# Performance work log

Measured on AMD Instinct MI355X. Metric: run time of the kernel, lower is better.

The kernel has to match this reference:

```python
import jax, jax.numpy as jnp
import numpy as np

DIM = 768
HEADS = 12
DH = DIM // HEADS
HIDDEN = 4 * DIM
EPS = 1e-5


def layernorm(x, g, b):
    mu = jnp.mean(x, axis=-1, keepdims=True)
    var = jnp.mean(jnp.square(x - mu), axis=-1, keepdims=True)
    return (x - mu) * jax.lax.rsqrt(var + EPS) * g + b


def setup_inputs() -> dict:
    key = jax.random.key(0)
    ks = jax.random.split(key, 12)
    B, N = 8, 1024
    s_in = 1.0 / np.sqrt(DIM)
    s_hid = 1.0 / np.sqrt(HIDDEN)
    return {
        "x": jax.random.normal(ks[0], (B, N, DIM), jnp.float32),
        "q_extra": jax.random.normal(ks[1], (B, N, DIM), jnp.float32),
        "ln1_g": jnp.ones((DIM,), jnp.float32),
        "ln1_b": jnp.zeros((DIM,), jnp.float32),
        "w_kv": jax.random.normal(ks[2], (DIM, 2 * DIM), jnp.float32) * s_in,
        "w_out": jax.random.normal(ks[3], (DIM, DIM), jnp.float32) * s_in,
        "b_out": jnp.zeros((DIM,), jnp.float32),
        "ln2_g": jnp.ones((DIM,), jnp.float32),
        "ln2_b": jnp.zeros((DIM,), jnp.float32),
        "w1": jax.random.normal(ks[4], (DIM, HIDDEN), jnp.float32) * s_in,
        "b1": jnp.zeros((HIDDEN,), jnp.float32),
        "w2": jax.random.normal(ks[5], (HIDDEN, DIM), jnp.float32) * s_hid,
        "b2": jnp.zeros((DIM,), jnp.float32),
    }


def reference(x, q_extra, ln1_g, ln1_b, w_kv, w_out, b_out, ln2_g, ln2_b, w1, b1, w2, b2):
    B, N, C = x.shape
    scale = DH ** (-0.5)

    # pre-norm cross attention
    xn = layernorm(x, ln1_g, ln1_b)
    kv = (xn @ w_kv).reshape(B, N, 2, HEADS, DH)
    k = kv[:, :, 0]  # [B,N,H,Dh]
    v = kv[:, :, 1]
    q = q_extra.reshape(B, N, HEADS, DH)
    dots = jnp.einsum('bnhd,bmhd->bhnm', q, k) * scale
    attn = jax.nn.softmax(dots, axis=-1)
    out = jnp.einsum('bhnm,bmhd->bnhd', attn, v).reshape(B, N, C)
    out = out @ w_out + b_out

    x = x + out  # residual

    # pre-norm MLP
    h = layernorm(x, ln2_g, ln2_b)
    h = jax.nn.gelu(h @ w1 + b1, approximate=False)
    h = h @ w2 + b2
    return x + h
```

## Files before the change

### kernel.cpp

```cpp
#include <hip/hip_runtime.h>

typedef __attribute__((ext_vector_type(8))) short short8;
typedef __attribute__((ext_vector_type(8))) _Float16 half8;
typedef __attribute__((ext_vector_type(2))) __fp16 fp16x2;
typedef __attribute__((ext_vector_type(4))) float float4v;

__device__ __forceinline__ unsigned short f2bf(float f) {
  union { unsigned int i; float f; } x; x.f = f;
  unsigned int r = x.i + 0x7fffu + ((x.i >> 16) & 1u);
  return (unsigned short)(r >> 16);
}

__global__ void ln_kernel(const float* __restrict__ in, const float* __restrict__ g,
                          const float* __restrict__ b, unsigned short* __restrict__ out) {
  const int row = blockIdx.x, t = threadIdx.x;
  const float* xr = in + (size_t)row * 768;
  float v0 = xr[t], v1 = xr[t + 256], v2 = xr[t + 512];
  float s = v0 + v1 + v2;
  float s2 = v0 * v0 + v1 * v1 + v2 * v2;
  for (int off = 32; off > 0; off >>= 1) {
    s += __shfl_xor(s, off, 64);
    s2 += __shfl_xor(s2, off, 64);
  }
  __shared__ float red[8];
  const int wave = t >> 6, lane = t & 63;
  if (lane == 0) { red[wave] = s; red[wave + 4] = s2; }
  __syncthreads();
  s = red[0] + red[1] + red[2] + red[3];
  s2 = red[4] + red[5] + red[6] + red[7];
  const float mu = s * (1.0f / 768.0f);
  const float var = s2 * (1.0f / 768.0f) - mu * mu;
  const float rstd = rsqrtf(var + 1e-5f);
  unsigned short* orow = out + (size_t)row * 768;
  orow[t]       = f2bf((v0 - mu) * rstd * g[t]       + b[t]);
  orow[t + 256] = f2bf((v1 - mu) * rstd * g[t + 256] + b[t + 256]);
  orow[t + 512] = f2bf((v2 - mu) * rstd * g[t + 512] + b[t + 512]);
}

__global__ void wtrans_kernel(const float* __restrict__ in, unsigned short* __restrict__ out,
                              int K, int N) {
  __shared__ float tile[32][33];
  const int k0 = blockIdx.y * 32, n0 = blockIdx.x * 32;
  const int tr = threadIdx.x >> 5, tc = threadIdx.x & 31;
#pragma unroll
  for (int i = 0; i < 4; ++i)
    tile[tr + i * 8][tc] = in[(size_t)(k0 + tr + i * 8) * N + n0 + tc];
  __syncthreads();
#pragma unroll
  for (int i = 0; i < 4; ++i)
    out[(size_t)(n0 + tr + i * 8) * K + k0 + tc] = f2bf(tile[tc][tr + i * 8]);
}

__device__ __forceinline__ void gemm128(
    const unsigned short* __restrict__ A, int lda,
    const unsigned short* __restrict__ Bt, int ldb, int K,
    int row0, int col0,
    unsigned short* As, unsigned short* Bs,
    float4v acc[4][4]) {
  const int t = threadIdx.x, lane = t & 63, wave = t >> 6;
  const int quad = lane >> 4, l16 = lane & 15;
  const int wr = wave >> 1, wc = wave & 1;
  const int sr = lane >> 2;
  const int sc = (lane & 3) * 8;
#pragma unroll
  for (int mt = 0; mt < 4; ++mt)
#pragma unroll
    for (int nt = 0; nt < 4; ++nt) acc[mt][nt] = (float4v)(0.0f);

  for (int kk = 0; kk < K; kk += 32) {
    __syncthreads();
#pragma unroll
    for (int j = 0; j < 2; ++j) {
      const int chunk = wave * 2 + j;
      const int r = chunk * 16 + sr;
      __builtin_amdgcn_global_load_lds(
          (const __attribute__((address_space(1))) unsigned int*)(A + (size_t)(row0 + r) * lda + kk + sc),
          (__attribute__((address_space(3))) unsigned int*)(As + chunk * 512),
          16, 0, 0);
      __builtin_amdgcn_global_load_lds(
          (const __attribute__((address_space(1))) unsigned int*)(Bt + (size_t)(col0 + r) * ldb + kk + sc),
          (__attribute__((address_space(3))) unsigned int*)(Bs + chunk * 512),
          16, 0, 0);
    }
    __syncthreads();
    short8 af[4], bfv[4];
#pragma unroll
    for (int i = 0; i < 4; ++i) {
      af[i]  = *(const short8*)(As + (wr * 64 + i * 16 + l16) * 32 + quad * 8);
      bfv[i] = *(const short8*)(Bs + (wc * 64 + i * 16 + l16) * 32 + quad * 8);
    }
#pragma unroll
    for (int mt = 0; mt < 4; ++mt)
#pragma unroll
      for (int nt = 0; nt < 4; ++nt)
        acc[mt][nt] = __builtin_amdgcn_mfma_f32_16x16x32_bf16(af[mt], bfv[nt], acc[mt][nt], 0, 0, 0);
  }
}

#define GEMM128_PROLOGUE                                         \
  __shared__ unsigned short As[128 * 32];                        \
  __shared__ unsigned short Bs[128 * 32];                        \
  float4v acc[4][4];                                             \
  const int col0 = blockIdx.x * 128, row0 = blockIdx.y * 128;    \
  const int t = threadIdx.x, lane = t & 63, wave = t >> 6;       \
  const int quad = lane >> 4, l16 = lane & 15;                   \
  const int wr = wave >> 1, wc = wave & 1; (void)t;

__device__ __forceinline__ void gemm12864(
    const unsigned short* __restrict__ A, int lda,
    const unsigned short* __restrict__ Bt, int ldb, int K,
    int row0, int col0,
    unsigned short* As, unsigned short* Bs,
    float4v acc[2][4]) {
  const int t = threadIdx.x, lane = t & 63, wave = t >> 6;
  const int quad = lane >> 4, l16 = lane & 15;
  const int sr = lane >> 2;
  const int sc = (lane & 3) * 8;
#pragma unroll
  for (int mt = 0; mt < 2; ++mt)
#pragma unroll
    for (int nt = 0; nt < 4; ++nt) acc[mt][nt] = (float4v)(0.0f);

  for (int kk = 0; kk < K; kk += 32) {
    __syncthreads();
#pragma unroll
    for (int j = 0; j < 2; ++j) {
      const int chunk = wave * 2 + j;
      const int r = chunk * 16 + sr;
      __builtin_amdgcn_global_load_lds(
          (const __attribute__((address_space(1))) unsigned int*)(A + (size_t)(row0 + r) * lda + kk + sc),
          (__attribute__((address_space(3))) unsigned int*)(As + chunk * 512),
          16, 0, 0);
    }
    {
      const int r = wave * 16 + sr;
      __builtin_amdgcn_global_load_lds(
          (const __attribute__((address_space(1))) unsigned int*)(Bt + (size_t)(col0 + r) * ldb + kk + sc),
          (__attribute__((address_space(3))) unsigned int*)(Bs + wave * 512),
          16, 0, 0);
    }
    __syncthreads();
    short8 af[2], bfv[4];
#pragma unroll
    for (int i = 0; i < 2; ++i)
      af[i] = *(const short8*)(As + (wave * 32 + i * 16 + l16) * 32 + quad * 8);
#pragma unroll
    for (int i = 0; i < 4; ++i)
      bfv[i] = *(const short8*)(Bs + (i * 16 + l16) * 32 + quad * 8);
#pragma unroll
    for (int mt = 0; mt < 2; ++mt)
#pragma unroll
      for (int nt = 0; nt < 4; ++nt)
        acc[mt][nt] = __builtin_amdgcn_mfma_f32_16x16x32_bf16(af[mt], bfv[nt], acc[mt][nt], 0, 0, 0);
  }
}

#define GEMM12864_PROLOGUE                                       \
  __shared__ unsigned short As[128 * 32];                        \
  __shared__ unsigned short Bs[64 * 32];                         \
  float4v acc[2][4];                                             \
  const int col0 = blockIdx.x * 64, row0 = blockIdx.y * 128;     \
  const int t = threadIdx.x, lane = t & 63, wave = t >> 6;       \
  const int quad = lane >> 4, l16 = lane & 15; (void)t;

__global__ void gemm_kv_kernel(const unsigned short* __restrict__ xn,
                               const unsigned short* __restrict__ wkvt,
                               _Float16* __restrict__ kbuf,
                               _Float16* __restrict__ vtbuf) {
  GEMM128_PROLOGUE
  gemm128(xn, 768, wkvt, 768, 768, row0, col0, As, Bs, acc);
#pragma unroll
  for (int mt = 0; mt < 4; ++mt)
#pragma unroll
    for (int nt = 0; nt < 4; ++nt) {
      const int j = col0 + wc * 64 + nt * 16 + l16;
#pragma unroll
      for (int r = 0; r < 4; ++r) {
        const int m = row0 + wr * 64 + mt * 16 + quad * 4 + r;
        const int bb = m >> 10, n = m & 1023;
        const float c = acc[mt][nt][r];
        if (j < 768) {
          const int hh = j >> 6, d = j & 63;
          kbuf[((size_t)(bb * 12 + hh) * 1024 + n) * 64 + d] = (_Float16)c;
        } else {
          const int j2 = j - 768, hh = j2 >> 6, d = j2 & 63;
          vtbuf[((size_t)(bb * 12 + hh) * 64 + d) * 1024 + n] = (_Float16)c;
        }
      }
    }
}

#define AST 72
#define PST 72
__global__ void attn_kernel(const float* __restrict__ q_extra,
                            const _Float16* __restrict__ kbuf,
                            const _Float16* __restrict__ vtbuf,
                            unsigned short* __restrict__ ao) {
  __shared__ _Float16 Ks[64 * AST];
  __shared__ _Float16 Vs[64 * AST];
  __shared__ _Float16 Ps[4][2][16 * PST];
  const int b = blockIdx.z, h = blockIdx.y, q0 = blockIdx.x * 128;
  const int t = threadIdx.x, lane = t & 63, wave = t >> 6;
  const int quad = lane >> 4, l16 = lane & 15;

  half8 qf[2][2];
#pragma unroll
  for (int qt = 0; qt < 2; ++qt) {
    const float* qp = q_extra +
        ((size_t)((b * 1024 + q0 + qt * 64 + wave * 16 + l16) * 12 + h)) * 64 + quad * 8;
    float4 a0 = *(const float4*)(qp);
    float4 a1 = *(const float4*)(qp + 4);
    float4 c0 = *(const float4*)(qp + 32);
    float4 c1 = *(const float4*)(qp + 36);
    union { fp16x2 h2[4]; half8 h8; } u0, u1;
    u0.h2[0] = __builtin_amdgcn_cvt_pkrtz(a0.x * 0.125f, a0.y * 0.125f);
    u0.h2[1] = __builtin_amdgcn_cvt_pkrtz(a0.z * 0.125f, a0.w * 0.125f);
    u0.h2[2] = __builtin_amdgcn_cvt_pkrtz(a1.x * 0.125f, a1.y * 0.125f);
    u0.h2[3] = __builtin_amdgcn_cvt_pkrtz(a1.z * 0.125f, a1.w * 0.125f);
    u1.h2[0] = __builtin_amdgcn_cvt_pkrtz(c0.x * 0.125f, c0.y * 0.125f);
    u1.h2[1] = __builtin_amdgcn_cvt_pkrtz(c0.z * 0.125f, c0.w * 0.125f);
    u1.h2[2] = __builtin_amdgcn_cvt_pkrtz(c1.x * 0.125f, c1.y * 0.125f);
    u1.h2[3] = __builtin_amdgcn_cvt_pkrtz(c1.z * 0.125f, c1.w * 0.125f);
    qf[qt][0] = u0.h8; qf[qt][1] = u1.h8;
  }

  const _Float16* kb = kbuf + (size_t)(b * 12 + h) * 65536;
  const _Float16* vb = vtbuf + (size_t)(b * 12 + h) * 65536;
  const int srow = t >> 2, su = (t & 3) * 16;

  half8 kp0 = *(const half8*)(kb + (size_t)srow * 64 + su);
  half8 kp1 = *(const half8*)(kb + (size_t)srow * 64 + su + 8);
  half8 vp0 = *(const half8*)(vb + (size_t)srow * 1024 + su);
  half8 vp1 = *(const half8*)(vb + (size_t)srow * 1024 + su + 8);

  float m_s[2] = {-1e30f, -1e30f}, l_s[2] = {0.f, 0.f};
  float4v acc[2][4];
#pragma unroll
  for (int qt = 0; qt < 2; ++qt)
#pragma unroll
    for (int nt = 0; nt < 4; ++nt) acc[qt][nt] = (float4v)(0.f);

  for (int c = 0; c < 16; ++c) {
    __syncthreads();
    *(half8*)(Ks + srow * AST + su)     = kp0;
    *(half8*)(Ks + srow * AST + su + 8) = kp1;
    *(half8*)(Vs + srow * AST + su)     = vp0;
    *(half8*)(Vs + srow * AST + su + 8) = vp1;
    if (c < 15) {
      const int key1 = (c + 1) * 64;
      kp0 = *(const half8*)(kb + (size_t)(key1 + srow) * 64 + su);
      kp1 = *(const half8*)(kb + (size_t)(key1 + srow) * 64 + su + 8);
      vp0 = *(const half8*)(vb + (size_t)srow * 1024 + key1 + su);
      vp1 = *(const half8*)(vb + (size_t)srow * 1024 + key1 + su + 8);
    }
    __syncthreads();

    float4v s[2][4];
#pragma unroll
    for (int kt = 0; kt < 4; ++kt) {
      const _Float16* kr = Ks + (kt * 16 + l16) * AST;
      half8 kf0 = *(const half8*)(kr + quad * 8);
      half8 kf1 = *(const half8*)(kr + 32 + quad * 8);
#pragma unroll
      for (int qt = 0; qt < 2; ++qt) {
        float4v a = (float4v)(0.f);
        a = __builtin_amdgcn_mfma_f32_16x16x32_f16(kf0, qf[qt][0], a, 0, 0, 0);
        a = __builtin_amdgcn_mfma_f32_16x16x32_f16(kf1, qf[qt][1], a, 0, 0, 0);
        s[qt][kt] = a;
      }
    }

    float ab[2][4];
#pragma unroll
    for (int qt = 0; qt < 2; ++qt) {
      float mx = fmaxf(fmaxf(fmaxf(s[qt][0][0], s[qt][0][1]), fmaxf(s[qt][0][2], s[qt][0][3])),
                       fmaxf(fmaxf(s[qt][1][0], s[qt][1][1]), fmaxf(s[qt][1][2], s[qt][1][3])));
      mx = fmaxf(mx, fmaxf(fmaxf(fmaxf(s[qt][2][0], s[qt][2][1]), fmaxf(s[qt][2][2], s[qt][2][3])),
                           fmaxf(fmaxf(s[qt][3][0], s[qt][3][1]), fmaxf(s[qt][3][2], s[qt][3][3]))));
      mx = fmaxf(mx, __shfl_xor(mx, 16, 64));
      mx = fmaxf(mx, __shfl_xor(mx, 32, 64));
      const float mn = fmaxf(m_s[qt], mx);
      const float alpha = __expf(m_s[qt] - mn);
      m_s[qt] = mn;
      _Float16* pw = Ps[wave][qt];
      float sum = 0.0f;
#pragma unroll
      for (int kt = 0; kt < 4; ++kt) {
        const float p0 = __expf(s[qt][kt][0] - mn);
        const float p1 = __expf(s[qt][kt][1] - mn);
        const float p2 = __expf(s[qt][kt][2] - mn);
        const float p3 = __expf(s[qt][kt][3] - mn);
        sum += (p0 + p1) + (p2 + p3);
        union { fp16x2 h2[2]; uint2 u; } pk;
        pk.h2[0] = __builtin_amdgcn_cvt_pkrtz(p0, p1);
        pk.h2[1] = __builtin_amdgcn_cvt_pkrtz(p2, p3);
        *(uint2*)(pw + l16 * PST + kt * 16 + quad * 4) = pk.u;
      }
      sum += __shfl_xor(sum, 16, 64);
      sum += __shfl_xor(sum, 32, 64);
      l_s[qt] = l_s[qt] * alpha + sum;
#pragma unroll
      for (int r = 0; r < 4; ++r) ab[qt][r] = __shfl(alpha, quad * 4 + r, 64);
#pragma unroll
      for (int nt = 0; nt < 4; ++nt)
#pragma unroll
        for (int r = 0; r < 4; ++r) acc[qt][nt][r] *= ab[qt][r];
    }

    half8 pf[2][2];
#pragma unroll
    for (int qt = 0; qt < 2; ++qt) {
      const _Float16* pw = Ps[wave][qt];
      pf[qt][0] = *(const half8*)(pw + l16 * PST + quad * 8);
      pf[qt][1] = *(const half8*)(pw + l16 * PST + 32 + quad * 8);
    }
#pragma unroll
    for (int nt = 0; nt < 4; ++nt) {
      const _Float16* vr = Vs + (nt * 16 + l16) * AST;
      half8 vf0 = *(const half8*)(vr + quad * 8);
      half8 vf1 = *(const half8*)(vr + 32 + quad * 8);
#pragma unroll
      for (int qt = 0; qt < 2; ++qt) {
        acc[qt][nt] = __builtin_amdgcn_mfma_f32_16x16x32_f16(pf[qt][0], vf0, acc[qt][nt], 0, 0, 0);
        acc[qt][nt] = __builtin_amdgcn_mfma_f32_16x16x32_f16(pf[qt][1], vf1, acc[qt][nt], 0, 0, 0);
      }
    }
  }

#pragma unroll
  for (int qt = 0; qt < 2; ++qt) {
    const float inv = 1.0f / l_s[qt];
    float ib[4];
#pragma unroll
    for (int r = 0; r < 4; ++r) ib[r] = __shfl(inv, quad * 4 + r, 64);
#pragma unroll
    for (int nt = 0; nt < 4; ++nt) {
#pragma unroll
      for (int r = 0; r < 4; ++r) {
        const int m = q0 + qt * 64 + wave * 16 + quad * 4 + r;
        ao[(size_t)(b * 1024 + m) * 768 + h * 64 + nt * 16 + l16] =
            f2bf(acc[qt][nt][r] * ib[r]);
      }
    }
  }
}

__global__ void gemm_outproj_kernel(const unsigned short* __restrict__ ao,
                                    const unsigned short* __restrict__ woutt,
                                    const float* __restrict__ b_out,
                                    const float* __restrict__ x,
                                    float* __restrict__ x2) {
  GEMM12864_PROLOGUE
  gemm12864(ao, 768, woutt, 768, 768, row0, col0, As, Bs, acc);
#pragma unroll
  for (int mt = 0; mt < 2; ++mt)
#pragma unroll
    for (int nt = 0; nt < 4; ++nt) {
      const int j = col0 + nt * 16 + l16;
#pragma unroll
      for (int r = 0; r < 4; ++r) {
        const int m = row0 + wave * 32 + mt * 16 + quad * 4 + r;
        const size_t idx = (size_t)m * 768 + j;
        x2[idx] = acc[mt][nt][r] + b_out[j] + x[idx];
      }
    }
}

__global__ void gemm_mlp1_kernel(const unsigned short* __restrict__ h,
                                 const unsigned short* __restrict__ w1t,
                                 const float* __restrict__ b1,
                                 unsigned short* __restrict__ h1) {
  GEMM128_PROLOGUE
  gemm128(h, 768, w1t, 768, 768, row0, col0, As, Bs, acc);
#pragma unroll
  for (int mt = 0; mt < 4; ++mt)
#pragma unroll
    for (int nt = 0; nt < 4; ++nt) {
      const int j = col0 + wc * 64 + nt * 16 + l16;
#pragma unroll
      for (int r = 0; r < 4; ++r) {
        const int m = row0 + wr * 64 + mt * 16 + quad * 4 + r;
        const float y = acc[mt][nt][r] + b1[j];
        const float ge = 0.5f * y * (1.0f + erff(y * 0.70710678118654752f));
        h1[(size_t)m * 3072 + j] = f2bf(ge);
      }
    }
}

__global__ void gemm_mlp2_kernel(const unsigned short* __restrict__ h1,
                                 const unsigned short* __restrict__ w2t,
                                 const float* __restrict__ b2,
                                 const float* __restrict__ x2,
                                 float* __restrict__ out) {
  GEMM12864_PROLOGUE
  gemm12864(h1, 3072, w2t, 3072, 3072, row0, col0, As, Bs, acc);
#pragma unroll
  for (int mt = 0; mt < 2; ++mt)
#pragma unroll
    for (int nt = 0; nt < 4; ++nt) {
      const int j = col0 + nt * 16 + l16;
#pragma unroll
      for (int r = 0; r < 4; ++r) {
        const int m = row0 + wave * 32 + mt * 16 + quad * 4 + r;
        const size_t idx = (size_t)m * 768 + j;
        out[idx] = acc[mt][nt][r] + b2[j] + x2[idx];
      }
    }
}

extern "C" void kernel_launch(void* const* d_in, const int* in_sizes, int n_in,
                              void* d_out, int out_size, void* d_ws, size_t ws_size,
                              hipStream_t stream) {
  const float* x       = (const float*)d_in[0];
  const float* q_extra = (const float*)d_in[1];
  const float* ln1_g   = (const float*)d_in[2];
  const float* ln1_b   = (const float*)d_in[3];
  const float* w_kv    = (const float*)d_in[4];
  const float* w_out   = (const float*)d_in[5];
  const float* b_out   = (const float*)d_in[6];
  const float* ln2_g   = (const float*)d_in[7];
  const float* ln2_b   = (const float*)d_in[8];
  const float* w1      = (const float*)d_in[9];
  const float* b1      = (const float*)d_in[10];
  const float* w2      = (const float*)d_in[11];
  const float* b2      = (const float*)d_in[12];
  float* out = (float*)d_out;

  char* ws = (char*)d_ws;
  unsigned short* xn    = (unsigned short*)(ws);
  _Float16*       kbuf  = (_Float16*)(ws + 12582912);
  _Float16*       vtbuf = (_Float16*)(ws + 25165824);
  unsigned short* ao    = (unsigned short*)(ws + 37748736);
  float*          x2    = (float*)(ws + 50331648);
  unsigned short* h1    = (unsigned short*)(ws + 75497472);
  unsigned short* hbuf  = xn;
  unsigned short* wkvt  = ao;
  unsigned short* woutt = h1;
  unsigned short* w1t   = (unsigned short*)kbuf;
  unsigned short* w2t   = (unsigned short*)vtbuf;

  ln_kernel<<<8192, 256, 0, stream>>>(x, ln1_g, ln1_b, xn);
  wtrans_kernel<<<dim3(48, 24), 256, 0, stream>>>(w_kv, wkvt, 768, 1536);
  wtrans_kernel<<<dim3(24, 24), 256, 0, stream>>>(w_out, woutt, 768, 768);
  gemm_kv_kernel<<<dim3(12, 64), 256, 0, stream>>>(xn, wkvt, kbuf, vtbuf);
  attn_kernel<<<dim3(8, 12, 8), 256, 0, stream>>>(q_extra, kbuf, vtbuf, ao);
  wtrans_kernel<<<dim3(96, 24), 256, 0, stream>>>(w1, w1t, 768, 3072);
  wtrans_kernel<<<dim3(24, 96), 256, 0, stream>>>(w2, w2t, 3072, 768);
  gemm_outproj_kernel<<<dim3(12, 64), 256, 0, stream>>>(ao, woutt, b_out, x, x2);
  ln_kernel<<<8192, 256, 0, stream>>>(x2, ln2_g, ln2_b, hbuf);
  gemm_mlp1_kernel<<<dim3(24, 64), 256, 0, stream>>>(hbuf, w1t, b1, h1);
  gemm_mlp2_kernel<<<dim3(12, 64), 256, 0, stream>>>(h1, w2t, b2, x2, out);
}
```

Before: 429.4 us.

## Deepen GEMM K-tile to 64, XOR-swizzle LDS, and remap blocks per XCD

The GEMM helpers now stage 64-wide K tiles instead of 32, which halves the number of barrier-separated loop iterations. LDS columns are XOR-swizzled by row so the fragment reads avoid bank conflicts. All GEMM launches move to 1D grids, and a swizzle maps consecutive block IDs on the same XCD to contiguous row bands, aiming for better L2 reuse. Shared memory per block doubles, which may reduce occupancy.

Measured after the change: 389.7 us. 9.3% less time.

```diff
diff --git a/kernel.cpp b/kernel.cpp
--- a/kernel.cpp
+++ b/kernel.cpp
@@ -51,6 +51,13 @@
     out[(size_t)(n0 + tr + i * 8) * K + k0 + tc] = f2bf(tile[tc][tr + i * 8]);
 }
 
+#define SWIZ_BLOCK(GX, TW)                                        \
+  const int _id = (int)blockIdx.x;                                \
+  const int _gy8 = (int)gridDim.x / (8 * (GX));                   \
+  const int _xcd = _id & 7, _jj = _id >> 3;                       \
+  const int row0 = (_xcd * _gy8 + _jj / (GX)) * 128;              \
+  const int col0 = (_jj % (GX)) * (TW);
+
 __device__ __forceinline__ void gemm128(
     const unsigned short* __restrict__ A, int lda,
     const unsigned short* __restrict__ Bt, int ldb, int K,
@@ -60,48 +67,52 @@
   const int t = threadIdx.x, lane = t & 63, wave = t >> 6;
   const int quad = lane >> 4, l16 = lane & 15;
   const int wr = wave >> 1, wc = wave & 1;
-  const int sr = lane >> 2;
-  const int sc = (lane & 3) * 8;
+  const int srow = lane >> 3;
+  const int scol = ((lane & 7) ^ srow) * 8;
 #pragma unroll
   for (int mt = 0; mt < 4; ++mt)
 #pragma unroll
     for (int nt = 0; nt < 4; ++nt) acc[mt][nt] = (float4v)(0.0f);
 
-  for (int kk = 0; kk < K; kk += 32) {
-    __syncthreads();
-#pragma unroll
-    for (int j = 0; j < 2; ++j) {
-      const int chunk = wave * 2 + j;
-      const int r = chunk * 16 + sr;
+  for (int kk = 0; kk < K; kk += 64) {
+    __syncthreads();
+#pragma unroll
+    for (int j = 0; j < 4; ++j) {
+      const int chunk = wave * 4 + j;
+      const int r = chunk * 8 + srow;
       __builtin_amdgcn_global_load_lds(
-          (const __attribute__((address_space(1))) unsigned int*)(A + (size_t)(row0 + r) * lda + kk + sc),
+          (const __attribute__((address_space(1))) unsigned int*)(A + (size_t)(row0 + r) * lda + kk + scol),
           (__attribute__((address_space(3))) unsigned int*)(As + chunk * 512),
           16, 0, 0);
       __builtin_amdgcn_global_load_lds(
-          (const __attribute__((address_space(1))) unsigned int*)(Bt + (size_t)(col0 + r) * ldb + kk + sc),
+          (const __attribute__((address_space(1))) unsigned int*)(Bt + (size_t)(col0 + r) * ldb + kk + scol),
           (__attribute__((address_space(3))) unsigned int*)(Bs + chunk * 512),
           16, 0, 0);
     }
     __syncthreads();
-    short8 af[4], bfv[4];
-#pragma unroll
-    for (int i = 0; i < 4; ++i) {
-      af[i]  = *(const short8*)(As + (wr * 64 + i * 16 + l16) * 32 + quad * 8);
-      bfv[i] = *(const short8*)(Bs + (wc * 64 + i * 16 + l16) * 32 + quad * 8);
-    }
-#pragma unroll
-    for (int mt = 0; mt < 4; ++mt)
-#pragma unroll
-      for (int nt = 0; nt < 4; ++nt)
-        acc[mt][nt] = __builtin_amdgcn_mfma_f32_16x16x32_bf16(af[mt], bfv[nt], acc[mt][nt], 0, 0, 0);
-  }
-}
-
-#define GEMM128_PROLOGUE                                         \
-  __shared__ unsigned short As[128 * 32];                        \
-  __shared__ unsigned short Bs[128 * 32];                        \
+#pragma unroll
+    for (int ks = 0; ks < 2; ++ks) {
+      const int gsw = ((ks * 4 + quad) ^ (l16 & 7)) * 8;
+      short8 af[4], bfv[4];
+#pragma unroll
+      for (int i = 0; i < 4; ++i) {
+        af[i]  = *(const short8*)(As + (wr * 64 + i * 16 + l16) * 64 + gsw);
+        bfv[i] = *(const short8*)(Bs + (wc * 64 + i * 16 + l16) * 64 + gsw);
+      }
+#pragma unroll
+      for (int mt = 0; mt < 4; ++mt)
+#pragma unroll
+        for (int nt = 0; nt < 4; ++nt)
+          acc[mt][nt] = __builtin_amdgcn_mfma_f32_16x16x32_bf16(af[mt], bfv[nt], acc[mt][nt], 0, 0, 0);
+    }
+  }
+}
+
+#define GEMM128_PROLOGUE(GX)                                     \
+  __shared__ unsigned short As[128 * 64];                        \
+  __shared__ unsigned short Bs[128 * 64];                        \
   float4v acc[4][4];                                             \
-  const int col0 = blockIdx.x * 128, row0 = blockIdx.y * 128;    \
+  SWIZ_BLOCK(GX, 128)                                            \
   const int t = threadIdx.x, lane = t & 63, wave = t >> 6;       \
   const int quad = lane >> 4, l16 = lane & 15;                   \
   const int wr = wave >> 1, wc = wave & 1; (void)t;
@@ -114,52 +125,58 @@
     float4v acc[2][4]) {
   const int t = threadIdx.x, lane = t & 63, wave = t >> 6;
   const int quad = lane >> 4, l16 = lane & 15;
-  const int sr = lane >> 2;
-  const int sc = (lane & 3) * 8;
+  const int srow = lane >> 3;
+  const int scol = ((lane & 7) ^ srow) * 8;
 #pragma unroll
   for (int mt = 0; mt < 2; ++mt)
 #pragma unroll
     for (int nt = 0; nt < 4; ++nt) acc[mt][nt] = (float4v)(0.0f);
 
-  for (int kk = 0; kk < K; kk += 32) {
-    __syncthreads();
+  for (int kk = 0; kk < K; kk += 64) {
+    __syncthreads();
+#pragma unroll
+    for (int j = 0; j < 4; ++j) {
+      const int chunk = wave * 4 + j;
+      const int r = chunk * 8 + srow;
+      __builtin_amdgcn_global_load_lds(
+          (const __attribute__((address_space(1))) unsigned int*)(A + (size_t)(row0 + r) * lda + kk + scol),
+          (__attribute__((address_space(3))) unsigned int*)(As + chunk * 512),
+          16, 0, 0);
+    }
 #pragma unroll
     for (int j = 0; j < 2; ++j) {
       const int chunk = wave * 2 + j;
-      const int r = chunk * 16 + sr;
+      const int r = chunk * 8 + srow;
       __builtin_amdgcn_global_load_lds(
-          (const __attribute__((address_space(1))) unsigned int*)(A + (size_t)(row0 + r) * lda + kk + sc),
-          (__attribute__((address_space(3))) unsigned int*)(As + chunk * 512),
+          (const __attribute__((address_space(1))) unsigned int*)(Bt + (size_t)(col0 + r) * ldb + kk + scol),
+          (__attribute__((address_space(3))) unsigned int*)(Bs + chunk * 512),
           16, 0, 0);
     }
-    {
-      const int r = wave * 16 + sr;
-      __builtin_amdgcn_global_load_lds(
-          (const __attribute__((address_space(1))) unsigned int*)(Bt + (size_t)(col0 + r) * ldb + kk + sc),
-          (__attribute__((address_space(3))) unsigned int*)(Bs + wave * 512),
-          16, 0, 0);
-    }
-    __syncthreads();
-    short8 af[2], bfv[4];
-#pragma unroll
-    for (int i = 0; i < 2; ++i)
-      af[i] = *(const short8*)(As + (wave * 32 + i * 16 + l16) * 32 + quad * 8);
-#pragma unroll
-    for (int i = 0; i < 4; ++i)
-      bfv[i] = *(const short8*)(Bs + (i * 16 + l16) * 32 + quad * 8);
-#pragma unroll
-    for (int mt = 0; mt < 2; ++mt)
-#pragma unroll
-      for (int nt = 0; nt < 4; ++nt)
-        acc[mt][nt] = __builtin_amdgcn_mfma_f32_16x16x32_bf16(af[mt], bfv[nt], acc[mt][nt], 0, 0, 0);
-  }
-}
-
-#define GEMM12864_PROLOGUE                                       \
-  __shared__ unsigned short As[128 * 32];                        \
-  __shared__ unsigned short Bs[64 * 32];                         \
+    __syncthreads();
+#pragma unroll
+    for (int ks = 0; ks < 2; ++ks) {
+      const int gsw = ((ks * 4 + quad) ^ (l16 & 7)) * 8;
+      short8 af[2], bfv[4];
+#pragma unroll
+      for (int i = 0; i < 2; ++i)
+        af[i] = *(const short8*)(As + (wave * 32 + i * 16 + l16) * 64 + gsw);
+#pragma unroll
+      for (int i = 0; i < 4; ++i)
+        bfv[i] = *(const short8*)(Bs + (i * 16 + l16) * 64 + gsw);
+#pragma unroll
+      for (int mt = 0; mt < 2; ++mt)
+#pragma unroll
+        for (int nt = 0; nt < 4; ++nt)
+          acc[mt][nt] = __builtin_amdgcn_mfma_f32_16x16x32_bf16(af[mt], bfv[nt], acc[mt][nt], 0, 0, 0);
+    }
+  }
+}
+
+#define GEMM12864_PROLOGUE(GX)                                   \
+  __shared__ unsigned short As[128 * 64];                        \
+  __shared__ unsigned short Bs[64 * 64];                         \
   float4v acc[2][4];                                             \
-  const int col0 = blockIdx.x * 64, row0 = blockIdx.y * 128;     \
+  SWIZ_BLOCK(GX, 64)                                             \
   const int t = threadIdx.x, lane = t & 63, wave = t >> 6;       \
   const int quad = lane >> 4, l16 = lane & 15; (void)t;
 
@@ -167,7 +184,7 @@
                                const unsigned short* __restrict__ wkvt,
                                _Float16* __restrict__ kbuf,
                                _Float16* __restrict__ vtbuf) {
-  GEMM128_PROLOGUE
+  GEMM128_PROLOGUE(12)
   gemm128(xn, 768, wkvt, 768, 768, row0, col0, As, Bs, acc);
 #pragma unroll
   for (int mt = 0; mt < 4; ++mt)
@@ -350,7 +367,7 @@
                                     const float* __restrict__ b_out,
                                     const float* __restrict__ x,
                                     float* __restrict__ x2) {
-  GEMM12864_PROLOGUE
+  GEMM12864_PROLOGUE(12)
   gemm12864(ao, 768, woutt, 768, 768, row0, col0, As, Bs, acc);
 #pragma unroll
   for (int mt = 0; mt < 2; ++mt)
@@ -370,7 +387,7 @@
                                  const unsigned short* __restrict__ w1t,
                                  const float* __restrict__ b1,
                                  unsigned short* __restrict__ h1) {
-  GEMM128_PROLOGUE
+  GEMM128_PROLOGUE(24)
   gemm128(h, 768, w1t, 768, 768, row0, col0, As, Bs, acc);
 #pragma unroll
   for (int mt = 0; mt < 4; ++mt)
@@ -392,7 +409,7 @@
                                  const float* __restrict__ b2,
                                  const float* __restrict__ x2,
                                  float* __restrict__ out) {
-  GEMM12864_PROLOGUE
+  GEMM12864_PROLOGUE(12)
   gemm12864(h1, 3072, w2t, 3072, 3072, row0, col0, As, Bs, acc);
 #pragma unroll
   for (int mt = 0; mt < 2; ++mt)
@@ -442,12 +459,12 @@
   ln_kernel<<<8192, 256, 0, stream>>>(x, ln1_g, ln1_b, xn);
   wtrans_kernel<<<dim3(48, 24), 256, 0, stream>>>(w_kv, wkvt, 768, 1536);
   wtrans_kernel<<<dim3(24, 24), 256, 0, stream>>>(w_out, woutt, 768, 768);
-  gemm_kv_kernel<<<dim3(12, 64), 256, 0, stream>>>(xn, wkvt, kbuf, vtbuf);
+  gemm_kv_kernel<<<768, 256, 0, stream>>>(xn, wkvt, kbuf, vtbuf);
   attn_kernel<<<dim3(8, 12, 8), 256, 0, stream>>>(q_extra, kbuf, vtbuf, ao);
   wtrans_kernel<<<dim3(96, 24), 256, 0, stream>>>(w1, w1t, 768, 3072);
   wtrans_kernel<<<dim3(24, 96), 256, 0, stream>>>(w2, w2t, 3072, 768);
-  gemm_outproj_kernel<<<dim3(12, 64), 256, 0, stream>>>(ao, woutt, b_out, x, x2);
+  gemm_outproj_kernel<<<768, 256, 0, stream>>>(ao, woutt, b_out, x, x2);
   ln_kernel<<<8192, 256, 0, stream>>>(x2, ln2_g, ln2_b, hbuf);
-  gemm_mlp1_kernel<<<dim3(24, 64), 256, 0, stream>>>(hbuf, w1t, b1, h1);
-  gemm_mlp2_kernel<<<dim3(12, 64), 256, 0, stream>>>(h1, w2t, b2, x2, out);
-}
+  gemm_mlp1_kernel<<<1536, 256, 0, stream>>>(hbuf, w1t, b1, h1);
+  gemm_mlp2_kernel<<<768, 256, 0, stream>>>(h1, w2t, b2, x2, out);
+}
```
